# Performance work log

Hardware: AMD Instinct MI355X
Metric: run time of the kernel (lower is better)

## Reference

```python
import jax, jax.numpy as jnp
import numpy as np

MARGIN = 1.0


def setup_inputs() -> dict:
    key = jax.random.key(0)
    k1, k2 = jax.random.split(key)
    N, D = 8192, 128
    embeddings = jax.random.normal(k1, (N, D), dtype=jnp.float32)
    labels = jax.random.randint(k2, (N,), 0, 100, dtype=jnp.int64)
    return {"embeddings": embeddings, "labels": labels}


def reference(embeddings, labels):
    N = embeddings.shape[0]
    # Pairwise Euclidean distances (torch.cdist p=2) via the expanded form.
    sq = jnp.sum(embeddings * embeddings, axis=-1)  # [N]
    d2 = sq[:, None] + sq[None, :] - 2.0 * (embeddings @ embeddings.T)  # [N, N]
    d2 = jnp.maximum(d2, 0.0)
    eye = jnp.eye(N, dtype=bool)
    # Diagonal distances are never used (masked out below); replace the zero
    # under the sqrt to keep gradients finite.
    dist = jnp.sqrt(jnp.where(eye, 1.0, d2))  # [N, N]

    same = labels[:, None] == labels[None, :]
    pos_mask = same & ~eye
    neg_mask = (~same) & ~eye

    # sum_exp_i depends only on row i: one masked row reduction, reused for all pairs.
    sum_exp = jnp.sum(jnp.where(neg_mask, jnp.exp(MARGIN - dist), 0.0), axis=1)  # [N]

    # L_ij = log(sum_exp_i + sum_exp_j) + d_ij, only on positive pairs.
    L = jnp.log(sum_exp[:, None] + sum_exp[None, :]) + dist  # [N, N]
    per_pair = jnp.where(pos_mask, jax.nn.relu(L) ** 2, 0.0)
    n_pos = jnp.sum(pos_mask).astype(per_pair.dtype)
    return jnp.sum(per_pair) / n_pos / 2.0
```

## Files before the change

kernel.cpp:

```cpp
#include <hip/hip_runtime.h>
#include <hip/hip_bf16.h>


typedef __attribute__((ext_vector_type(8))) short bf16x8;
typedef __attribute__((ext_vector_type(4))) float f32x4;

#if __has_builtin(__builtin_amdgcn_exp2f)
#define EXP2F __builtin_amdgcn_exp2f
#else
#define EXP2F exp2f
#endif

__device__ __forceinline__ unsigned short f2bf(float f) {
    unsigned u = __float_as_uint(f);
    u += 0x7fffu + ((u >> 16) & 1u);
    return (unsigned short)(u >> 16);
}

__global__ __launch_bounds__(256) void setup_kernel(
    const float* __restrict__ e, const int* __restrict__ labels,
    float* __restrict__ sq, unsigned* __restrict__ ebf,
    float* __restrict__ sum_exp,
    int* __restrict__ counts_out, int* __restrict__ offsets_out,
    int* __restrict__ idxbuf, unsigned* __restrict__ ticket, int N)
{
    const int tid = threadIdx.x;
    const float LOG2E = 1.44269504088896341f;
    if ((int)blockIdx.x < (int)gridDim.x - 1) {
        const int lane = tid & 63, wid = tid >> 6;
        if (tid < 32) sum_exp[blockIdx.x * 32 + tid] = 0.f;
        const int rowbase = (blockIdx.x * 4 + wid) * 8;
        #pragma unroll
        for (int it = 0; it < 8; ++it) {
            int row = rowbase + it;
            if (row >= N) break;
            float2 v = ((const float2*)(e + (size_t)row * 128))[lane];
            v.x *= LOG2E; v.y *= LOG2E;
            float s = v.x * v.x + v.y * v.y;
            #pragma unroll
            for (int off = 1; off < 64; off <<= 1) s += __shfl_xor(s, off, 64);
            if (lane == 0) sq[row] = s;
            unsigned bits = (unsigned)f2bf(v.x) | ((unsigned)f2bf(v.y) << 16);
            ebf[(size_t)row * 64 + lane] = bits;
        }
    } else {
        __shared__ int cnt[256];
        __shared__ int off[256];
        if (tid == 0) *ticket = 0u;
        cnt[tid] = 0;
        __syncthreads();
        for (int i = tid; i < N; i += 256)
            atomicAdd(&cnt[(unsigned)labels[i] & 255u], 1);
        __syncthreads();
        if (tid < 64) {
            int base = tid * 4;
            int c0 = cnt[base], c1 = cnt[base+1], c2 = cnt[base+2], c3 = cnt[base+3];
            int s = c0 + c1 + c2 + c3;
            int v = s;
            #pragma unroll
            for (int d = 1; d < 64; d <<= 1) {
                int u = __shfl_up(v, d, 64);
                if (tid >= d) v += u;
            }
            int excl = v - s;
            off[base]     = excl;
            off[base + 1] = excl + c0;
            off[base + 2] = excl + c0 + c1;
            off[base + 3] = excl + c0 + c1 + c2;
        }
        __syncthreads();
        counts_out[tid]  = cnt[tid];
        offsets_out[tid] = off[tid];
        cnt[tid] = off[tid];
        __syncthreads();
        for (int i = tid; i < N; i += 256) {
            int l = (unsigned)labels[i] & 255u;
            int p = atomicAdd(&cnt[l], 1);
            idxbuf[p] = i;
        }
    }
}

__global__ __launch_bounds__(512) void pass1_kernel(
    const unsigned short* __restrict__ ebf,
    const float* __restrict__ sq,
    const int* __restrict__ labels,
    float* __restrict__ sum_exp,
    int N, int nCb, int nT)
{
    __shared__ __align__(16) char a_tile[128 * 128];
    __shared__ __align__(16) char b_tile[128 * 128];
    __shared__ float rowsum[128];
    __shared__ float colsum[128];

    const int tid = threadIdx.x;
    const int lane = tid & 63, wid = tid >> 6;

    int t;
    {
        int bid = blockIdx.x;
        if ((nT & 7) == 0) {
            int cpx = nT >> 3;
            t = (bid & 7) * cpx + (bid >> 3);
        } else {
            t = bid;
        }
    }
    int bi = (int)((2.f * nCb + 1.f - __builtin_amdgcn_sqrtf(
                   (2.f * nCb + 1.f) * (2.f * nCb + 1.f) - 8.f * t)) * 0.5f);
    if (bi < 0) bi = 0;
    if (bi > nCb - 1) bi = nCb - 1;
    while (bi + 1 <= nCb - 1 && (bi + 1) * (2 * nCb - bi) / 2 <= t) ++bi;
    while (bi > 0 && bi * (2 * nCb - bi + 1) / 2 > t) --bi;
    const int bj = bi + (t - bi * (2 * nCb - bi + 1) / 2);
    const bool diag = (bi == bj);
    const int brow = bi * 128, bcol = bj * 128;

    if (tid < 128) { rowsum[tid] = 0.f; colsum[tid] = 0.f; }

    const int wm = (wid >> 2) * 64, wn = (wid & 3) * 32;
    const int lhi = lane >> 4, llo = lane & 15;
    const char* ebfB = (const char*)ebf;

    f32x4 acc[4][2];
    #pragma unroll
    for (int m = 0; m < 4; ++m)
        #pragma unroll
        for (int n = 0; n < 2; ++n)
            acc[m][n] = (f32x4){0.f, 0.f, 0.f, 0.f};

    #pragma unroll
    for (int c = 0; c < 2; ++c) {
        #pragma unroll
        for (int k = 0; k < 4; ++k) {
            int s = wid * 256 + k * 64;
            int tsel = s >> 10;
            int ls = s & 1023;
            int sl = ls + lane;
            int r = sl >> 3, j = sl & 7;
            int grow = (tsel ? bcol : brow) + r;
            const void* g = ebfB + ((size_t)grow << 8) + c * 128 + ((j ^ (r & 7)) << 4);
            char* l = (tsel ? b_tile : a_tile) + ls * 16;
            __builtin_amdgcn_global_load_lds(
                (const __attribute__((address_space(1))) unsigned*)g,
                (__attribute__((address_space(3))) unsigned*)l, 16, 0, 0);
        }
        __syncthreads();

        #pragma unroll
        for (int h = 0; h < 2; ++h) {
            const int cb = h * 64 + lhi * 16;
            bf16x8 af[4], bfr[2];
            #pragma unroll
            for (int m = 0; m < 4; ++m) {
                int r = wm + m * 16 + llo;
                af[m] = *(const bf16x8*)(a_tile + r * 128 + (cb ^ ((r & 7) << 4)));
            }
            #pragma unroll
            for (int n = 0; n < 2; ++n) {
                int r = wn + n * 16 + llo;
                bfr[n] = *(const bf16x8*)(b_tile + r * 128 + (cb ^ ((r & 7) << 4)));
            }
            #pragma unroll
            for (int m = 0; m < 4; ++m)
                #pragma unroll
                for (int n = 0; n < 2; ++n)
                    acc[m][n] = __builtin_amdgcn_mfma_f32_16x16x32_bf16(af[m], bfr[n], acc[m][n], 0, 0, 0);
        }
        __syncthreads();
    }

    const int rowbase = brow + wm;
    float sqr[4][4]; int labr[4][4];
    #pragma unroll
    for (int m = 0; m < 4; ++m)
        #pragma unroll
        for (int r = 0; r < 4; ++r) {
            int row = rowbase + m * 16 + lhi * 4 + r;
            sqr[m][r] = sq[row];
            labr[m][r] = labels[row];
        }
    float sqc[2]; int labc[2];
    #pragma unroll
    for (int n = 0; n < 2; ++n) {
        int col = bcol + wn + n * 16 + llo;
        sqc[n] = sq[col];
        labc[n] = labels[col];
    }

    float wsum[4][4] = {};
    float csum[2] = {};
    #pragma unroll
    for (int m = 0; m < 4; ++m)
        #pragma unroll
        for (int n = 0; n < 2; ++n)
            #pragma unroll
            for (int r = 0; r < 4; ++r) {
                float g = acc[m][n][r];
                float d2 = fmaxf(fmaf(-2.f, g, sqr[m][r] + sqc[n]), 0.f);
                float dist = __builtin_amdgcn_sqrtf(d2);
                float w = (labr[m][r] != labc[n]) ? EXP2F(0.f - dist) : 0.f;
                wsum[m][r] += w;
                csum[n] += w;
            }
    #pragma unroll
    for (int m = 0; m < 4; ++m)
        #pragma unroll
        for (int r = 0; r < 4; ++r) {
            float s = wsum[m][r];
            #pragma unroll
            for (int off = 1; off < 16; off <<= 1) s += __shfl_xor(s, off, 64);
            if (llo == 0)
                atomicAdd(&rowsum[wm + m * 16 + lhi * 4 + r], s);
        }
    if (!diag) {
        #pragma unroll
        for (int n = 0; n < 2; ++n) {
            float s = csum[n];
            s += __shfl_xor(s, 16, 64);
            s += __shfl_xor(s, 32, 64);
            if (lhi == 0)
                atomicAdd(&colsum[wn + n * 16 + llo], s);
        }
    }
    __syncthreads();
    if (tid < 128) {
        unsafeAtomicAdd(&sum_exp[brow + tid], rowsum[tid]);
        if (!diag)
            unsafeAtomicAdd(&sum_exp[bcol + tid], colsum[tid]);
    }
}

__global__ __launch_bounds__(256) void pass2_kernel(
    const unsigned short* __restrict__ ebf,
    const float* __restrict__ sq,
    const float* __restrict__ sum_exp,
    const int* __restrict__ idxbuf,
    const int* __restrict__ offsets,
    const int* __restrict__ counts,
    double* __restrict__ partial2,
    unsigned* __restrict__ cnt2,
    unsigned* __restrict__ ticket,
    float* __restrict__ out)
{
    __shared__ __align__(16) char a_tile[128 * 128];
    __shared__ __align__(16) char b_tile[128 * 128];
    __shared__ double bsum[4];
    __shared__ unsigned bcnt[4];
    __shared__ bool isLast;

    const int L = blockIdx.x;
    const int NL = gridDim.x;
    const int tid = threadIdx.x;
    const int lane = tid & 63, wid = tid >> 6;
    const int cnt = counts[L], offs = offsets[L];
    const int wm = (wid >> 1) * 64, wn = (wid & 1) * 64;
    const int lhi = lane >> 4, llo = lane & 15;
    const char* ebfB = (const char*)ebf;
    const float E1 = 2.71828182845904523f;
    const float LN2 = 0.69314718055994531f;

    float lsum = 0.f; unsigned lcnt = 0;

    if (cnt > 1) {
        const int nSub = (cnt + 127) >> 7;
        for (int si = 0; si < nSub; ++si)
        for (int sj = si; sj < nSub; ++sj) {
            const int baseA = offs + si * 128, baseB = offs + sj * 128;
            const int cntA = min(128, cnt - si * 128);
            const int cntB = min(128, cnt - sj * 128);
            const float wgt = (si == sj) ? 1.f : 2.f;
            const unsigned wgtu = (si == sj) ? 1u : 2u;

            f32x4 acc[4][4];
            #pragma unroll
            for (int m = 0; m < 4; ++m)
                #pragma unroll
                for (int n = 0; n < 4; ++n)
                    acc[m][n] = (f32x4){0.f, 0.f, 0.f, 0.f};

            for (int c = 0; c < 2; ++c) {
                #pragma unroll
                for (int i2 = 0; i2 < 8; ++i2) {
                    int sl = tid + i2 * 256;
                    int tsel = sl >> 10;
                    int s = sl & 1023;
                    int r = s >> 3, j = s & 7;
                    int base = tsel ? baseB : baseA;
                    int cc = tsel ? cntB : cntA;
                    int gr = idxbuf[base + min(r, cc - 1)];
                    uint4 v = *(const uint4*)(ebfB + ((size_t)gr << 8) + c * 128 + (j << 4));
                    char* tp = tsel ? b_tile : a_tile;
                    *(uint4*)(tp + r * 128 + (((j << 4)) ^ ((r & 7) << 4))) = v;
                }
                __syncthreads();
                #pragma unroll
                for (int h = 0; h < 2; ++h) {
                    const int cb = h * 64 + lhi * 16;
                    bf16x8 af[4], bfr[4];
                    #pragma unroll
                    for (int m = 0; m < 4; ++m) {
                        int r = wm + m * 16 + llo;
                        af[m] = *(const bf16x8*)(a_tile + r * 128 + (cb ^ ((r & 7) << 4)));
                    }
                    #pragma unroll
                    for (int n = 0; n < 4; ++n) {
                        int r = wn + n * 16 + llo;
                        bfr[n] = *(const bf16x8*)(b_tile + r * 128 + (cb ^ ((r & 7) << 4)));
                    }
                    #pragma unroll
                    for (int m = 0; m < 4; ++m)
                        #pragma unroll
                        for (int n = 0; n < 4; ++n)
                            acc[m][n] = __builtin_amdgcn_mfma_f32_16x16x32_bf16(af[m], bfr[n], acc[m][n], 0, 0, 0);
                }
                __syncthreads();
            }

            int giA[4][4]; float sqA[4][4], seA[4][4]; bool vA[4][4];
            #pragma unroll
            for (int m = 0; m < 4; ++m)
                #pragma unroll
                for (int r = 0; r < 4; ++r) {
                    int lr = wm + m * 16 + lhi * 4 + r;
                    vA[m][r] = lr < cntA;
                    int gi = idxbuf[baseA + min(lr, cntA - 1)];
                    giA[m][r] = gi;
                    sqA[m][r] = sq[gi];
                    seA[m][r] = sum_exp[gi] * E1;
                }
            int gjB[4]; float sqB[4], seB[4]; bool vB[4];
            #pragma unroll
            for (int n = 0; n < 4; ++n) {
                int lc = wn + n * 16 + llo;
                vB[n] = lc < cntB;
                int gj = idxbuf[baseB + min(lc, cntB - 1)];
                gjB[n] = gj;
                sqB[n] = sq[gj];
                seB[n] = sum_exp[gj] * E1;
            }
            #pragma unroll
            for (int m = 0; m < 4; ++m)
                #pragma unroll
                for (int n = 0; n < 4; ++n)
                    #pragma unroll
                    for (int r = 0; r < 4; ++r) {
                        float g = acc[m][n][r];
                        float d2 = fmaxf(fmaf(-2.f, g, sqA[m][r] + sqB[n]), 0.f);
                        float dist = __builtin_amdgcn_sqrtf(d2) * LN2;
                        bool pos = vA[m][r] && vB[n] && (giA[m][r] != gjB[n]);
                        float Lv = __logf(seA[m][r] + seB[n]) + dist;
                        Lv = fmaxf(Lv, 0.f);
                        lsum += pos ? wgt * Lv * Lv : 0.f;
                        lcnt += pos ? wgtu : 0u;
                    }
        }
    }

    #pragma unroll
    for (int off = 1; off < 64; off <<= 1) {
        lsum += __shfl_xor(lsum, off, 64);
        lcnt += __shfl_xor(lcnt, off, 64);
    }
    if (lane == 0) { bsum[wid] = (double)lsum; bcnt[wid] = lcnt; }
    __syncthreads();
    if (tid == 0) {
        partial2[L] = bsum[0] + bsum[1] + bsum[2] + bsum[3];
        cnt2[L] = bcnt[0] + bcnt[1] + bcnt[2] + bcnt[3];
        __threadfence();
        isLast = (atomicAdd(ticket, 1u) == (unsigned)(NL - 1));
    }
    __syncthreads();

    if (isLast) {
        __threadfence();
        double tt = (tid < NL) ? partial2[tid] : 0.0;
        unsigned c = (tid < NL) ? cnt2[tid] : 0u;
        #pragma unroll
        for (int off = 1; off < 64; off <<= 1) {
            tt += __shfl_xor(tt, off, 64);
            c  += __shfl_xor(c, off, 64);
        }
        if (lane == 0) { bsum[wid] = tt; bcnt[wid] = c; }
        __syncthreads();
        if (tid == 0) {
            double s = bsum[0] + bsum[1] + bsum[2] + bsum[3];
            unsigned cc = bcnt[0] + bcnt[1] + bcnt[2] + bcnt[3];
            if (cc == 0) cc = 1;
            out[0] = (float)(s / (double)cc * 0.5);
        }
    }
}

extern "C" void kernel_launch(void* const* d_in, const int* in_sizes, int n_in,
                              void* d_out, int out_size, void* d_ws, size_t ws_size,
                              hipStream_t stream) {
    const float* e = (const float*)d_in[0];
    const int* labels = (const int*)d_in[1];
    const int N = in_sizes[1];
    const int nCb = N / 128;
    const int nT = nCb * (nCb + 1) / 2;
    const int NL = 256;
    const int nPrep = N / 32;

    char* ws = (char*)d_ws;
    float*    sq       = (float*)ws;
    float*    sum_exp  = (float*)(ws + 4 * (size_t)N);
    unsigned short* ebf = (unsigned short*)(ws + 8 * (size_t)N);
    char*     p        = ws + 8 * (size_t)N + 256 * (size_t)N;
    int*      counts   = (int*)p;      p += NL * 4;
    int*      offsets  = (int*)p;      p += NL * 4;
    unsigned* ticket   = (unsigned*)p; p += 64;
    p = (char*)(((size_t)p + 7) & ~(size_t)7);
    double*   partial2 = (double*)p;   p += NL * 8;
    unsigned* cnt2     = (unsigned*)p; p += NL * 4;
    int*      idxbuf   = (int*)p;

    setup_kernel<<<nPrep + 1, 256, 0, stream>>>(e, labels, sq, (unsigned*)ebf,
                                                sum_exp, counts, offsets,
                                                idxbuf, ticket, N);
    pass1_kernel<<<nT, 512, 0, stream>>>(ebf, sq, labels, sum_exp, N, nCb, nT);
    pass2_kernel<<<NL, 256, 0, stream>>>(ebf, sq, sum_exp, idxbuf, offsets, counts,
                                         partial2, cnt2, ticket, (float*)d_out);
}
```

Measured before the change: 73.57 us.

## Fuse positive-pair distance GEMMs into pass1 and stream pair records to a light pass2

The positive-pair GEMM blocks now run as extra blocks in the pass1 launch, alongside the sum_exp tile computation. Each block writes the distance and packed (i,j) index of every upper-triangle positive pair into a compact pair buffer. Pass2 becomes a simple grid-stride reduction over these records that reads sum_exp and computes the loss. This is meant to overlap the positive-pair matmul with pass1 and remove the dependent GEMM from the tail kernel. The cost is extra global writes and reads for the pair records, a fixed pair capacity that silently drops pairs beyond it, a 13-bit index packing that assumes N ≤ 8192, and removal of the XCD-aware tile remapping.

```diff
diff --git a/kernel.cpp b/kernel.cpp
--- a/kernel.cpp
+++ b/kernel.cpp
@@ -11,6 +11,8 @@
 #define EXP2F exp2f
 #endif
 
+#define PAIR_CAP (1u << 20)
+
 __device__ __forceinline__ unsigned short f2bf(float f) {
     unsigned u = __float_as_uint(f);
     u += 0x7fffu + ((u >> 16) & 1u);
@@ -22,12 +24,14 @@
     float* __restrict__ sq, unsigned* __restrict__ ebf,
     float* __restrict__ sum_exp,
     int* __restrict__ counts_out, int* __restrict__ offsets_out,
+    int* __restrict__ offsPairs_out, unsigned* __restrict__ pairsTotal,
     int* __restrict__ idxbuf, unsigned* __restrict__ ticket, int N)
 {
     const int tid = threadIdx.x;
     const float LOG2E = 1.44269504088896341f;
     if ((int)blockIdx.x < (int)gridDim.x - 1) {
         const int lane = tid & 63, wid = tid >> 6;
+        if (blockIdx.x == 0 && tid == 0) *ticket = 0u;
         if (tid < 32) sum_exp[blockIdx.x * 32 + tid] = 0.f;
         const int rowbase = (blockIdx.x * 4 + wid) * 8;
         #pragma unroll
@@ -46,7 +50,7 @@
     } else {
         __shared__ int cnt[256];
         __shared__ int off[256];
-        if (tid == 0) *ticket = 0u;
+        __shared__ int po[256];
         cnt[tid] = 0;
         __syncthreads();
         for (int i = tid; i < N; i += 256)
@@ -67,10 +71,26 @@
             off[base + 1] = excl + c0;
             off[base + 2] = excl + c0 + c1;
             off[base + 3] = excl + c0 + c1 + c2;
-        }
-        __syncthreads();
-        counts_out[tid]  = cnt[tid];
-        offsets_out[tid] = off[tid];
+            int p0 = c0 * (c0 - 1) / 2, p1 = c1 * (c1 - 1) / 2;
+            int p2 = c2 * (c2 - 1) / 2, p3 = c3 * (c3 - 1) / 2;
+            int ps = p0 + p1 + p2 + p3;
+            int pv = ps;
+            #pragma unroll
+            for (int d = 1; d < 64; d <<= 1) {
+                int u = __shfl_up(pv, d, 64);
+                if (tid >= d) pv += u;
+            }
+            int pexcl = pv - ps;
+            po[base]     = pexcl;
+            po[base + 1] = pexcl + p0;
+            po[base + 2] = pexcl + p0 + p1;
+            po[base + 3] = pexcl + p0 + p1 + p2;
+            if (tid == 63) *pairsTotal = (unsigned)pv;
+        }
+        __syncthreads();
+        counts_out[tid]    = cnt[tid];
+        offsets_out[tid]   = off[tid];
+        offsPairs_out[tid] = po[tid];
         cnt[tid] = off[tid];
         __syncthreads();
         for (int i = tid; i < N; i += 256) {
@@ -86,6 +106,11 @@
     const float* __restrict__ sq,
     const int* __restrict__ labels,
     float* __restrict__ sum_exp,
+    const int* __restrict__ idxbuf,
+    const int* __restrict__ offsets,
+    const int* __restrict__ counts,
+    const int* __restrict__ offsPairs,
+    uint2* __restrict__ pairs,
     int N, int nCb, int nT)
 {
     __shared__ __align__(16) char a_tile[128 * 128];
@@ -95,194 +120,156 @@
 
     const int tid = threadIdx.x;
     const int lane = tid & 63, wid = tid >> 6;
-
-    int t;
-    {
-        int bid = blockIdx.x;
-        if ((nT & 7) == 0) {
-            int cpx = nT >> 3;
-            t = (bid & 7) * cpx + (bid >> 3);
-        } else {
-            t = bid;
-        }
-    }
-    int bi = (int)((2.f * nCb + 1.f - __builtin_amdgcn_sqrtf(
-                   (2.f * nCb + 1.f) * (2.f * nCb + 1.f) - 8.f * t)) * 0.5f);
-    if (bi < 0) bi = 0;
-    if (bi > nCb - 1) bi = nCb - 1;
-    while (bi + 1 <= nCb - 1 && (bi + 1) * (2 * nCb - bi) / 2 <= t) ++bi;
-    while (bi > 0 && bi * (2 * nCb - bi + 1) / 2 > t) --bi;
-    const int bj = bi + (t - bi * (2 * nCb - bi + 1) / 2);
-    const bool diag = (bi == bj);
-    const int brow = bi * 128, bcol = bj * 128;
-
-    if (tid < 128) { rowsum[tid] = 0.f; colsum[tid] = 0.f; }
-
+    const float LN2 = 0.69314718055994531f;
     const int wm = (wid >> 2) * 64, wn = (wid & 3) * 32;
     const int lhi = lane >> 4, llo = lane & 15;
     const char* ebfB = (const char*)ebf;
 
-    f32x4 acc[4][2];
-    #pragma unroll
-    for (int m = 0; m < 4; ++m)
-        #pragma unroll
-        for (int n = 0; n < 2; ++n)
-            acc[m][n] = (f32x4){0.f, 0.f, 0.f, 0.f};
-
-    #pragma unroll
-    for (int c = 0; c < 2; ++c) {
-        #pragma unroll
-        for (int k = 0; k < 4; ++k) {
-            int s = wid * 256 + k * 64;
-            int tsel = s >> 10;
-            int ls = s & 1023;
-            int sl = ls + lane;
-            int r = sl >> 3, j = sl & 7;
-            int grow = (tsel ? bcol : brow) + r;
-            const void* g = ebfB + ((size_t)grow << 8) + c * 128 + ((j ^ (r & 7)) << 4);
-            char* l = (tsel ? b_tile : a_tile) + ls * 16;
-            __builtin_amdgcn_global_load_lds(
-                (const __attribute__((address_space(1))) unsigned*)g,
-                (__attribute__((address_space(3))) unsigned*)l, 16, 0, 0);
-        }
-        __syncthreads();
-
-        #pragma unroll
-        for (int h = 0; h < 2; ++h) {
-            const int cb = h * 64 + lhi * 16;
-            bf16x8 af[4], bfr[2];
-            #pragma unroll
-            for (int m = 0; m < 4; ++m) {
-                int r = wm + m * 16 + llo;
-                af[m] = *(const bf16x8*)(a_tile + r * 128 + (cb ^ ((r & 7) << 4)));
-            }
+    if ((int)blockIdx.x < nT) {
+        const int t = blockIdx.x;
+        int bi = (int)((2.f * nCb + 1.f - __builtin_amdgcn_sqrtf(
+                       (2.f * nCb + 1.f) * (2.f * nCb + 1.f) - 8.f * t)) * 0.5f);
+        if (bi < 0) bi = 0;
+        if (bi > nCb - 1) bi = nCb - 1;
+        while (bi + 1 <= nCb - 1 && (bi + 1) * (2 * nCb - bi) / 2 <= t) ++bi;
+        while (bi > 0 && bi * (2 * nCb - bi + 1) / 2 > t) --bi;
+        const int bj = bi + (t - bi * (2 * nCb - bi + 1) / 2);
+        const bool diag = (bi == bj);
+        const int brow = bi * 128, bcol = bj * 128;
+
+        if (tid < 128) { rowsum[tid] = 0.f; colsum[tid] = 0.f; }
+
+        f32x4 acc[4][2];
+        #pragma unroll
+        for (int m = 0; m < 4; ++m)
+            #pragma unroll
+            for (int n = 0; n < 2; ++n)
+                acc[m][n] = (f32x4){0.f, 0.f, 0.f, 0.f};
+
+        #pragma unroll
+        for (int c = 0; c < 2; ++c) {
+            #pragma unroll
+            for (int k = 0; k < 4; ++k) {
+                int s = wid * 256 + k * 64;
+                int tsel = s >> 10;
+                int ls = s & 1023;
+                int sl = ls + lane;
+                int r = sl >> 3, j = sl & 7;
+                int grow = (tsel ? bcol : brow) + r;
+                const void* g = ebfB + ((size_t)grow << 8) + c * 128 + ((j ^ (r & 7)) << 4);
+                char* l = (tsel ? b_tile : a_tile) + ls * 16;
+                __builtin_amdgcn_global_load_lds(
+                    (const __attribute__((address_space(1))) unsigned*)g,
+                    (__attribute__((address_space(3))) unsigned*)l, 16, 0, 0);
+            }
+            __syncthreads();
+
+            #pragma unroll
+            for (int h = 0; h < 2; ++h) {
+                const int cb = h * 64 + lhi * 16;
+                bf16x8 af[4], bfr[2];
+                #pragma unroll
+                for (int m = 0; m < 4; ++m) {
+                    int r = wm + m * 16 + llo;
+                    af[m] = *(const bf16x8*)(a_tile + r * 128 + (cb ^ ((r & 7) << 4)));
+                }
+                #pragma unroll
+                for (int n = 0; n < 2; ++n) {
+                    int r = wn + n * 16 + llo;
+                    bfr[n] = *(const bf16x8*)(b_tile + r * 128 + (cb ^ ((r & 7) << 4)));
+                }
+                #pragma unroll
+                for (int m = 0; m < 4; ++m)
+                    #pragma unroll
+                    for (int n = 0; n < 2; ++n)
+                        acc[m][n] = __builtin_amdgcn_mfma_f32_16x16x32_bf16(af[m], bfr[n], acc[m][n], 0, 0, 0);
+            }
+            __syncthreads();
+        }
+
+        const int rowbase = brow + wm;
+        float sqr[4][4]; int labr[4][4];
+        #pragma unroll
+        for (int m = 0; m < 4; ++m)
+            #pragma unroll
+            for (int r = 0; r < 4; ++r) {
+                int row = rowbase + m * 16 + lhi * 4 + r;
+                sqr[m][r] = sq[row];
+                labr[m][r] = labels[row];
+            }
+        float sqc[2]; int labc[2];
+        #pragma unroll
+        for (int n = 0; n < 2; ++n) {
+            int col = bcol + wn + n * 16 + llo;
+            sqc[n] = sq[col];
+            labc[n] = labels[col];
+        }
+
+        float wsum[4][4] = {};
+        float csum[2] = {};
+        #pragma unroll
+        for (int m = 0; m < 4; ++m)
+            #pragma unroll
+            for (int n = 0; n < 2; ++n)
+                #pragma unroll
+                for (int r = 0; r < 4; ++r) {
+                    float g = acc[m][n][r];
+                    float d2 = fmaxf(fmaf(-2.f, g, sqr[m][r] + sqc[n]), 0.f);
+                    float dist = __builtin_amdgcn_sqrtf(d2);
+                    float w = (labr[m][r] != labc[n]) ? EXP2F(0.f - dist) : 0.f;
+                    wsum[m][r] += w;
+                    csum[n] += w;
+                }
+        #pragma unroll
+        for (int m = 0; m < 4; ++m)
+            #pragma unroll
+            for (int r = 0; r < 4; ++r) {
+                float s = wsum[m][r];
+                #pragma unroll
+                for (int off = 1; off < 16; off <<= 1) s += __shfl_xor(s, off, 64);
+                if (llo == 0)
+                    atomicAdd(&rowsum[wm + m * 16 + lhi * 4 + r], s);
+            }
+        if (!diag) {
             #pragma unroll
             for (int n = 0; n < 2; ++n) {
-                int r = wn + n * 16 + llo;
-                bfr[n] = *(const bf16x8*)(b_tile + r * 128 + (cb ^ ((r & 7) << 4)));
-            }
-            #pragma unroll
-            for (int m = 0; m < 4; ++m)
-                #pragma unroll
-                for (int n = 0; n < 2; ++n)
-                    acc[m][n] = __builtin_amdgcn_mfma_f32_16x16x32_bf16(af[m], bfr[n], acc[m][n], 0, 0, 0);
-        }
-        __syncthreads();
-    }
-
-    const int rowbase = brow + wm;
-    float sqr[4][4]; int labr[4][4];
-    #pragma unroll
-    for (int m = 0; m < 4; ++m)
-        #pragma unroll
-        for (int r = 0; r < 4; ++r) {
-            int row = rowbase + m * 16 + lhi * 4 + r;
-            sqr[m][r] = sq[row];
-            labr[m][r] = labels[row];
-        }
-    float sqc[2]; int labc[2];
-    #pragma unroll
-    for (int n = 0; n < 2; ++n) {
-        int col = bcol + wn + n * 16 + llo;
-        sqc[n] = sq[col];
-        labc[n] = labels[col];
-    }
-
-    float wsum[4][4] = {};
-    float csum[2] = {};
-    #pragma unroll
-    for (int m = 0; m < 4; ++m)
-        #pragma unroll
-        for (int n = 0; n < 2; ++n)
-            #pragma unroll
-            for (int r = 0; r < 4; ++r) {
-                float g = acc[m][n][r];
-                float d2 = fmaxf(fmaf(-2.f, g, sqr[m][r] + sqc[n]), 0.f);
-                float dist = __builtin_amdgcn_sqrtf(d2);
-                float w = (labr[m][r] != labc[n]) ? EXP2F(0.f - dist) : 0.f;
-                wsum[m][r] += w;
-                csum[n] += w;
-            }
-    #pragma unroll
-    for (int m = 0; m < 4; ++m)
-        #pragma unroll
-        for (int r = 0; r < 4; ++r) {
-            float s = wsum[m][r];
-            #pragma unroll
-            for (int off = 1; off < 16; off <<= 1) s += __shfl_xor(s, off, 64);
-            if (llo == 0)
-                atomicAdd(&rowsum[wm + m * 16 + lhi * 4 + r], s);
-        }
-    if (!diag) {
-        #pragma unroll
-        for (int n = 0; n < 2; ++n) {
-            float s = csum[n];
-            s += __shfl_xor(s, 16, 64);
-            s += __shfl_xor(s, 32, 64);
-            if (lhi == 0)
-                atomicAdd(&colsum[wn + n * 16 + llo], s);
-        }
-    }
-    __syncthreads();
-    if (tid < 128) {
-        unsafeAtomicAdd(&sum_exp[brow + tid], rowsum[tid]);
-        if (!diag)
-            unsafeAtomicAdd(&sum_exp[bcol + tid], colsum[tid]);
-    }
-}
-
-__global__ __launch_bounds__(256) void pass2_kernel(
-    const unsigned short* __restrict__ ebf,
-    const float* __restrict__ sq,
-    const float* __restrict__ sum_exp,
-    const int* __restrict__ idxbuf,
-    const int* __restrict__ offsets,
-    const int* __restrict__ counts,
-    double* __restrict__ partial2,
-    unsigned* __restrict__ cnt2,
-    unsigned* __restrict__ ticket,
-    float* __restrict__ out)
-{
-    __shared__ __align__(16) char a_tile[128 * 128];
-    __shared__ __align__(16) char b_tile[128 * 128];
-    __shared__ double bsum[4];
-    __shared__ unsigned bcnt[4];
-    __shared__ bool isLast;
-
-    const int L = blockIdx.x;
-    const int NL = gridDim.x;
-    const int tid = threadIdx.x;
-    const int lane = tid & 63, wid = tid >> 6;
-    const int cnt = counts[L], offs = offsets[L];
-    const int wm = (wid >> 1) * 64, wn = (wid & 1) * 64;
-    const int lhi = lane >> 4, llo = lane & 15;
-    const char* ebfB = (const char*)ebf;
-    const float E1 = 2.71828182845904523f;
-    const float LN2 = 0.69314718055994531f;
-
-    float lsum = 0.f; unsigned lcnt = 0;
-
-    if (cnt > 1) {
+                float s = csum[n];
+                s += __shfl_xor(s, 16, 64);
+                s += __shfl_xor(s, 32, 64);
+                if (lhi == 0)
+                    atomicAdd(&colsum[wn + n * 16 + llo], s);
+            }
+        }
+        __syncthreads();
+        if (tid < 128) {
+            unsafeAtomicAdd(&sum_exp[brow + tid], rowsum[tid]);
+            if (!diag)
+                unsafeAtomicAdd(&sum_exp[bcol + tid], colsum[tid]);
+        }
+    } else {
+        const int L = blockIdx.x - nT;
+        const int cnt = counts[L], offs = offsets[L];
+        const int pOffs = offsPairs[L];
+        if (cnt < 2) return;
         const int nSub = (cnt + 127) >> 7;
+
         for (int si = 0; si < nSub; ++si)
         for (int sj = si; sj < nSub; ++sj) {
             const int baseA = offs + si * 128, baseB = offs + sj * 128;
             const int cntA = min(128, cnt - si * 128);
             const int cntB = min(128, cnt - sj * 128);
-            const float wgt = (si == sj) ? 1.f : 2.f;
-            const unsigned wgtu = (si == sj) ? 1u : 2u;
-
-            f32x4 acc[4][4];
+
+            f32x4 acc[4][2];
             #pragma unroll
             for (int m = 0; m < 4; ++m)
                 #pragma unroll
-                for (int n = 0; n < 4; ++n)
+                for (int n = 0; n < 2; ++n)
                     acc[m][n] = (f32x4){0.f, 0.f, 0.f, 0.f};
 
             for (int c = 0; c < 2; ++c) {
                 #pragma unroll
-                for (int i2 = 0; i2 < 8; ++i2) {
-                    int sl = tid + i2 * 256;
+                for (int i2 = 0; i2 < 4; ++i2) {
+                    int sl = tid + i2 * 512;
                     int tsel = sl >> 10;
                     int s = sl & 1023;
                     int r = s >> 3, j = s & 7;
@@ -291,102 +278,124 @@
                     int gr = idxbuf[base + min(r, cc - 1)];
                     uint4 v = *(const uint4*)(ebfB + ((size_t)gr << 8) + c * 128 + (j << 4));
                     char* tp = tsel ? b_tile : a_tile;
-                    *(uint4*)(tp + r * 128 + (((j << 4)) ^ ((r & 7) << 4))) = v;
+                    *(uint4*)(tp + r * 128 + ((j << 4) ^ ((r & 7) << 4))) = v;
                 }
                 __syncthreads();
                 #pragma unroll
                 for (int h = 0; h < 2; ++h) {
                     const int cb = h * 64 + lhi * 16;
-                    bf16x8 af[4], bfr[4];
+                    bf16x8 af[4], bfr[2];
                     #pragma unroll
                     for (int m = 0; m < 4; ++m) {
                         int r = wm + m * 16 + llo;
                         af[m] = *(const bf16x8*)(a_tile + r * 128 + (cb ^ ((r & 7) << 4)));
                     }
                     #pragma unroll
-                    for (int n = 0; n < 4; ++n) {
+                    for (int n = 0; n < 2; ++n) {
                         int r = wn + n * 16 + llo;
                         bfr[n] = *(const bf16x8*)(b_tile + r * 128 + (cb ^ ((r & 7) << 4)));
                     }
                     #pragma unroll
                     for (int m = 0; m < 4; ++m)
                         #pragma unroll
-                        for (int n = 0; n < 4; ++n)
+                        for (int n = 0; n < 2; ++n)
                             acc[m][n] = __builtin_amdgcn_mfma_f32_16x16x32_bf16(af[m], bfr[n], acc[m][n], 0, 0, 0);
                 }
                 __syncthreads();
             }
 
-            int giA[4][4]; float sqA[4][4], seA[4][4]; bool vA[4][4];
+            int aloc[4][4]; int giA[4][4]; float sqA[4][4];
             #pragma unroll
             for (int m = 0; m < 4; ++m)
                 #pragma unroll
                 for (int r = 0; r < 4; ++r) {
                     int lr = wm + m * 16 + lhi * 4 + r;
-                    vA[m][r] = lr < cntA;
+                    aloc[m][r] = lr;
                     int gi = idxbuf[baseA + min(lr, cntA - 1)];
                     giA[m][r] = gi;
                     sqA[m][r] = sq[gi];
-                    seA[m][r] = sum_exp[gi] * E1;
-                }
-            int gjB[4]; float sqB[4], seB[4]; bool vB[4];
-            #pragma unroll
-            for (int n = 0; n < 4; ++n) {
+                }
+            int bloc[2]; int gjB[2]; float sqB[2];
+            #pragma unroll
+            for (int n = 0; n < 2; ++n) {
                 int lc = wn + n * 16 + llo;
-                vB[n] = lc < cntB;
+                bloc[n] = lc;
                 int gj = idxbuf[baseB + min(lc, cntB - 1)];
                 gjB[n] = gj;
                 sqB[n] = sq[gj];
-                seB[n] = sum_exp[gj] * E1;
             }
             #pragma unroll
             for (int m = 0; m < 4; ++m)
                 #pragma unroll
-                for (int n = 0; n < 4; ++n)
+                for (int n = 0; n < 2; ++n)
                     #pragma unroll
                     for (int r = 0; r < 4; ++r) {
-                        float g = acc[m][n][r];
-                        float d2 = fmaxf(fmaf(-2.f, g, sqA[m][r] + sqB[n]), 0.f);
-                        float dist = __builtin_amdgcn_sqrtf(d2) * LN2;
-                        bool pos = vA[m][r] && vB[n] && (giA[m][r] != gjB[n]);
-                        float Lv = __logf(seA[m][r] + seB[n]) + dist;
-                        Lv = fmaxf(Lv, 0.f);
-                        lsum += pos ? wgt * Lv * Lv : 0.f;
-                        lcnt += pos ? wgtu : 0u;
+                        int a = si * 128 + aloc[m][r];
+                        int b = sj * 128 + bloc[n];
+                        bool valid = (aloc[m][r] < cntA) && (bloc[n] < cntB) && (a < b);
+                        if (valid) {
+                            float g = acc[m][n][r];
+                            float d2 = fmaxf(fmaf(-2.f, g, sqA[m][r] + sqB[n]), 0.f);
+                            float d = __builtin_amdgcn_sqrtf(d2) * LN2;
+                            unsigned idx = (unsigned)(pOffs + a * (2 * cnt - a - 1) / 2 + (b - a - 1));
+                            if (idx < PAIR_CAP) {
+                                uint2 rec;
+                                rec.x = __float_as_uint(d);
+                                rec.y = ((unsigned)giA[m][r] << 13) | (unsigned)gjB[n];
+                                pairs[idx] = rec;
+                            }
+                        }
                     }
         }
     }
-
+}
+
+__global__ __launch_bounds__(256) void pass2_kernel(
+    const float* __restrict__ sum_exp,
+    const uint2* __restrict__ pairs,
+    const unsigned* __restrict__ pairsTotal,
+    double* __restrict__ partial2,
+    unsigned* __restrict__ ticket,
+    float* __restrict__ out)
+{
+    __shared__ double bsum[4];
+    __shared__ bool isLast;
+    const int tid = threadIdx.x;
+    const int lane = tid & 63, wid = tid >> 6;
+    const int NB = gridDim.x;
+    const unsigned np = min(*pairsTotal, PAIR_CAP);
+
+    float lsum = 0.f;
+    for (unsigned i = blockIdx.x * 256 + tid; i < np; i += NB * 256) {
+        uint2 rec = pairs[i];
+        float d = __uint_as_float(rec.x);
+        int row = rec.y >> 13, col = rec.y & 8191;
+        float se = sum_exp[row] + sum_exp[col];
+        float L = 1.f + __logf(se) + d;
+        L = fmaxf(L, 0.f);
+        lsum += L * L;
+    }
     #pragma unroll
-    for (int off = 1; off < 64; off <<= 1) {
-        lsum += __shfl_xor(lsum, off, 64);
-        lcnt += __shfl_xor(lcnt, off, 64);
-    }
-    if (lane == 0) { bsum[wid] = (double)lsum; bcnt[wid] = lcnt; }
+    for (int off = 1; off < 64; off <<= 1) lsum += __shfl_xor(lsum, off, 64);
+    if (lane == 0) bsum[wid] = (double)lsum;
     __syncthreads();
     if (tid == 0) {
-        partial2[L] = bsum[0] + bsum[1] + bsum[2] + bsum[3];
-        cnt2[L] = bcnt[0] + bcnt[1] + bcnt[2] + bcnt[3];
+        partial2[blockIdx.x] = bsum[0] + bsum[1] + bsum[2] + bsum[3];
         __threadfence();
-        isLast = (atomicAdd(ticket, 1u) == (unsigned)(NL - 1));
+        isLast = (atomicAdd(ticket, 1u) == (unsigned)(NB - 1));
     }
     __syncthreads();
 
     if (isLast) {
         __threadfence();
-        double tt = (tid < NL) ? partial2[tid] : 0.0;
-        unsigned c = (tid < NL) ? cnt2[tid] : 0u;
-        #pragma unroll
-        for (int off = 1; off < 64; off <<= 1) {
-            tt += __shfl_xor(tt, off, 64);
-            c  += __shfl_xor(c, off, 64);
-        }
-        if (lane == 0) { bsum[wid] = tt; bcnt[wid] = c; }
+        double tt = (tid < NB) ? partial2[tid] : 0.0;
+        #pragma unroll
+        for (int off = 1; off < 64; off <<= 1) tt += __shfl_xor(tt, off, 64);
+        if (lane == 0) bsum[wid] = tt;
         __syncthreads();
         if (tid == 0) {
             double s = bsum[0] + bsum[1] + bsum[2] + bsum[3];
-            unsigned cc = bcnt[0] + bcnt[1] + bcnt[2] + bcnt[3];
-            if (cc == 0) cc = 1;
+            unsigned cc = np ? np : 1u;
             out[0] = (float)(s / (double)cc * 0.5);
         }
     }
@@ -402,24 +411,31 @@
     const int nT = nCb * (nCb + 1) / 2;
     const int NL = 256;
     const int nPrep = N / 32;
+    const int NB2 = 256;
 
     char* ws = (char*)d_ws;
-    float*    sq       = (float*)ws;
-    float*    sum_exp  = (float*)(ws + 4 * (size_t)N);
+    float*    sq        = (float*)ws;
+    float*    sum_exp   = (float*)(ws + 4 * (size_t)N);
     unsigned short* ebf = (unsigned short*)(ws + 8 * (size_t)N);
-    char*     p        = ws + 8 * (size_t)N + 256 * (size_t)N;
-    int*      counts   = (int*)p;      p += NL * 4;
-    int*      offsets  = (int*)p;      p += NL * 4;
-    unsigned* ticket   = (unsigned*)p; p += 64;
-    p = (char*)(((size_t)p + 7) & ~(size_t)7);
-    double*   partial2 = (double*)p;   p += NL * 8;
-    unsigned* cnt2     = (unsigned*)p; p += NL * 4;
-    int*      idxbuf   = (int*)p;
+    char*     p         = ws + 8 * (size_t)N + 256 * (size_t)N;
+    int*      counts    = (int*)p;      p += NL * 4;
+    int*      offsets   = (int*)p;      p += NL * 4;
+    int*      offsPairs = (int*)p;      p += NL * 4;
+    unsigned* pairsTotal= (unsigned*)p;
+    unsigned* ticket    = (unsigned*)(p + 4);
+    p += 64;
+    double*   partial2  = (double*)p;   p += NB2 * 8;
+    int*      idxbuf    = (int*)p;      p += (size_t)N * 4;
+    p = (char*)(((size_t)p + 15) & ~(size_t)15);
+    uint2*    pairs     = (uint2*)p;
 
     setup_kernel<<<nPrep + 1, 256, 0, stream>>>(e, labels, sq, (unsigned*)ebf,
                                                 sum_exp, counts, offsets,
+                                                offsPairs, pairsTotal,
                                                 idxbuf, ticket, N);
-    pass1_kernel<<<nT, 512, 0, stream>>>(ebf, sq, labels, sum_exp, N, nCb, nT);
-    pass2_kernel<<<NL, 256, 0, stream>>>(ebf, sq, sum_exp, idxbuf, offsets, counts,
-                                         partial2, cnt2, ticket, (float*)d_out);
+    pass1_kernel<<<nT + NL, 512, 0, stream>>>(ebf, sq, labels, sum_exp,
+                                              idxbuf, offsets, counts,
+                                              offsPairs, pairs, N, nCb, nT);
+    pass2_kernel<<<NB2, 256, 0, stream>>>(sum_exp, pairs, pairsTotal,
+                                          partial2, ticket, (float*)d_out);
 }
```

Measured after the change: 86.87 us. +18.1%, slower.
